# Kernel tuning notes

Hardware: AMD Instinct MI355X
Metric: run time of the kernel (lower is better)

## Reference

```python
import jax, jax.numpy as jnp
import numpy as np

EPS = 1e-5
SCALES = jnp.array([7.0, 7.0, 4.0], dtype=jnp.float32)  # (W, H, T) per source buffer
OUT_T, OUT_H, OUT_W = 3, 5, 5


def _roi_align3d(feat, start, end):
    """feat: [C,T,H,W]; start/end: [3] = (x, y, t). One sample per bin (bin center),
    trilinear interpolation, out-of-bounds -> 0 (standard ROIAlign convention)."""
    C, T, H, W = feat.shape
    dt = feat.dtype

    def centers(s, e, n):
        b = (e - s) / n
        return s + (jnp.arange(n, dtype=dt) + 0.5) * b

    xc = centers(start[0], end[0], OUT_W)  # [Wo]
    yc = centers(start[1], end[1], OUT_H)  # [Ho]
    tc = centers(start[2], end[2], OUT_T)  # [To]

    def prep(c, size):
        valid = ((c >= -1.0) & (c <= size)).astype(dt)
        c = jnp.clip(c, 0.0, size - 1)
        lo = jnp.floor(c).astype(jnp.int32)
        hi = jnp.minimum(lo + 1, size - 1)
        f = c - lo.astype(dt)
        return (lo, hi), ((1.0 - f) * valid, f * valid)

    ti, tw = prep(tc, T)
    yi, yw = prep(yc, H)
    xi, xw = prep(xc, W)

    out = jnp.zeros((C, OUT_T, OUT_H, OUT_W), dtype=dt)
    for a in range(2):
        for b in range(2):
            for c in range(2):
                g = feat[:, ti[a][:, None, None], yi[b][None, :, None], xi[c][None, None, :]]
                w = tw[a][:, None, None] * yw[b][None, :, None] * xw[c][None, None, :]
                out = out + g * w
    return out


def setup_inputs() -> dict:
    key = jax.random.key(0)
    k0, k1, k2 = jax.random.split(key, 3)
    B, C, T, H, W = 128, 1024, 4, 7, 7
    R = 256
    x = jax.random.normal(k0, (B, C, T, H, W), jnp.float32)
    w1 = jax.random.normal(k1, (R, C), jnp.float32) / np.sqrt(C).astype(np.float32)
    w2 = jax.random.normal(k2, (6, R), jnp.float32) / np.sqrt(R).astype(np.float32)
    return dict(
        x=x, w1=w1,
        g1=jnp.ones((R,), jnp.float32), b1=jnp.zeros((R,), jnp.float32),
        m1=jnp.zeros((R,), jnp.float32), v1=jnp.ones((R,), jnp.float32),
        w2=w2,
        g2=jnp.ones((6,), jnp.float32), b2=jnp.zeros((6,), jnp.float32),
        m2=jnp.zeros((6,), jnp.float32), v2=jnp.ones((6,), jnp.float32),
    )


def reference(x, w1, g1, b1, m1, v1, w2, g2, b2, m2, v2):
    # roi head: conv1x1x1 -> BN(eval) -> HSwish -> global avgpool -> conv1x1x1 -> BN(eval)
    h = jnp.einsum('bcthw,rc->brthw', x, w1)
    s1 = (g1 / jnp.sqrt(v1 + EPS))
    h = (h - m1[None, :, None, None, None]) * s1[None, :, None, None, None] + b1[None, :, None, None, None]
    h = h * jnp.clip(h + 3.0, 0.0, 6.0) * (1.0 / 6.0)  # HSwish
    h = h.mean(axis=(2, 3, 4))                          # AvgPool3d over full (T,H,W) -> [B,R]
    logits = h @ w2.T
    logits = (logits - m2) * (g2 / jnp.sqrt(v2 + EPS)) + b2  # [B,6]
    raw = jax.nn.sigmoid(logits)
    roi_start = 0.5 * raw[:, :3] * SCALES              # (x1,y1,t1)
    roi_end = (1.0 - 0.5 * raw[:, 3:]) * SCALES        # (x2,y2,t2)
    return jax.vmap(_roi_align3d)(x, roi_start, roi_end)  # [B,C,3,5,5]
```

## Files before the change

### kernel.cpp

```cpp
#include <hip/hip_runtime.h>

typedef __bf16 bf16x8 __attribute__((ext_vector_type(8)));
typedef float f32x4 __attribute__((ext_vector_type(4)));

#define EPS_F 1e-5f

__device__ __forceinline__ unsigned short f2bf(float f) {
    unsigned int u;
    __builtin_memcpy(&u, &f, 4);
    unsigned int r = (u + 0x7fffu + ((u >> 16) & 1u)) >> 16;
    return (unsigned short)r;
}

__global__ __launch_bounds__(256) void k_gemm_pool(
    const float* __restrict__ x,
    const float* __restrict__ w1,
    const float* __restrict__ g1,
    const float* __restrict__ b1,
    const float* __restrict__ m1,
    const float* __restrict__ v1,
    float* __restrict__ pooled)
{
    constexpr int LDK = 40;
    __shared__ unsigned short Alds[224 * LDK];
    __shared__ unsigned short Blds[64 * LDK];
    __shared__ float pool_lds[2][64];

    const int b   = blockIdx.x;
    const int r0  = blockIdx.y * 64;
    const int tid = threadIdx.x;
    const int wave = tid >> 6, lane = tid & 63;
    const int wn = wave >> 1, wm = wave & 1;
    const int q  = lane >> 4, ln = lane & 15;

    f32x4 acc[7][2];
#pragma unroll
    for (int i = 0; i < 7; i++)
#pragma unroll
        for (int j = 0; j < 2; j++) acc[i][j] = (f32x4){0.f, 0.f, 0.f, 0.f};

    const int c4 = tid / 28;
    const int p8 = tid % 28;

    for (int kc = 0; kc < 1024; kc += 32) {
        __syncthreads();
        {
            const int r  = tid >> 2;
            const int k8 = tid & 3;
            const float* wb = w1 + (size_t)(r0 + r) * 1024 + kc + k8 * 8;
            const float4 f0 = *(const float4*)wb;
            const float4 f1 = *(const float4*)(wb + 4);
            ushort4 o0, o1;
            o0.x = f2bf(f0.x); o0.y = f2bf(f0.y); o0.z = f2bf(f0.z); o0.w = f2bf(f0.w);
            o1.x = f2bf(f1.x); o1.y = f2bf(f1.y); o1.z = f2bf(f1.z); o1.w = f2bf(f1.w);
            *(ushort4*)&Blds[r * LDK + k8 * 8]     = o0;
            *(ushort4*)&Blds[r * LDK + k8 * 8 + 4] = o1;
        }
        if (tid < 224) {
            float rowv[4][8];
#pragma unroll
            for (int i = 0; i < 4; i++) {
                const int c = kc + c4 * 4 + i;
                const float* base = x + ((size_t)b * 1024 + c) * 196 + p8 * 8;
                if (p8 < 24) {
                    const float4 f0 = *(const float4*)base;
                    const float4 f1 = *(const float4*)(base + 4);
                    rowv[i][0] = f0.x; rowv[i][1] = f0.y; rowv[i][2] = f0.z; rowv[i][3] = f0.w;
                    rowv[i][4] = f1.x; rowv[i][5] = f1.y; rowv[i][6] = f1.z; rowv[i][7] = f1.w;
                } else if (p8 == 24) {
                    const float4 f0 = *(const float4*)base;
                    rowv[i][0] = f0.x; rowv[i][1] = f0.y; rowv[i][2] = f0.z; rowv[i][3] = f0.w;
                    rowv[i][4] = 0.f; rowv[i][5] = 0.f; rowv[i][6] = 0.f; rowv[i][7] = 0.f;
                } else {
#pragma unroll
                    for (int j = 0; j < 8; j++) rowv[i][j] = 0.f;
                }
            }
#pragma unroll
            for (int j = 0; j < 8; j++) {
                ushort4 o;
                o.x = f2bf(rowv[0][j]);
                o.y = f2bf(rowv[1][j]);
                o.z = f2bf(rowv[2][j]);
                o.w = f2bf(rowv[3][j]);
                *(ushort4*)&Alds[(p8 * 8 + j) * LDK + c4 * 4] = o;
            }
        }
        __syncthreads();
        bf16x8 bfr[2];
#pragma unroll
        for (int nt = 0; nt < 2; nt++)
            bfr[nt] = *(const bf16x8*)&Blds[(wn * 32 + nt * 16 + ln) * LDK + q * 8];
#pragma unroll
        for (int mi = 0; mi < 7; mi++) {
            const int mt = wm * 7 + mi;
            const bf16x8 af = *(const bf16x8*)&Alds[(mt * 16 + ln) * LDK + q * 8];
            acc[mi][0] = __builtin_amdgcn_mfma_f32_16x16x32_bf16(af, bfr[0], acc[mi][0], 0, 0, 0);
            acc[mi][1] = __builtin_amdgcn_mfma_f32_16x16x32_bf16(af, bfr[1], acc[mi][1], 0, 0, 0);
        }
    }

    float psum[2] = {0.f, 0.f};
#pragma unroll
    for (int nt = 0; nt < 2; nt++) {
        const int r = r0 + wn * 32 + nt * 16 + ln;
        const float s1 = g1[r] * rsqrtf(v1[r] + EPS_F);
        const float mu = m1[r];
        const float be = b1[r];
#pragma unroll
        for (int mi = 0; mi < 7; mi++) {
            const int mt = wm * 7 + mi;
#pragma unroll
            for (int i = 0; i < 4; i++) {
                const int m = mt * 16 + q * 4 + i;
                if (m < 196) {
                    float v = acc[mi][nt][i];
                    v = (v - mu) * s1 + be;
                    const float g = fminf(fmaxf(v + 3.f, 0.f), 6.f);
                    psum[nt] += v * g * (1.f / 6.f);
                }
            }
        }
    }
#pragma unroll
    for (int nt = 0; nt < 2; nt++) {
        psum[nt] += __shfl_xor(psum[nt], 16, 64);
        psum[nt] += __shfl_xor(psum[nt], 32, 64);
        if (lane < 16) pool_lds[wm][wn * 32 + nt * 16 + lane] = psum[nt];
    }
    __syncthreads();
    if (tid < 64)
        pooled[b * 256 + r0 + tid] =
            (pool_lds[0][tid] + pool_lds[1][tid]) * (1.f / 196.f);
}

__global__ __launch_bounds__(64) void k_logits(
    const float* __restrict__ pooled,
    const float* __restrict__ w2,
    const float* __restrict__ g2,
    const float* __restrict__ b2,
    const float* __restrict__ m2,
    const float* __restrict__ v2,
    float* __restrict__ roi)
{
    const int b = blockIdx.x, t = threadIdx.x;
    const float4 p4 = ((const float4*)(pooled + b * 256))[t];
    float part[6];
#pragma unroll
    for (int j = 0; j < 6; j++) {
        const float4 w = *(const float4*)(w2 + j * 256 + t * 4);
        part[j] = p4.x * w.x + p4.y * w.y + p4.z * w.z + p4.w * w.w;
    }
#pragma unroll
    for (int j = 0; j < 6; j++)
#pragma unroll
        for (int off = 32; off >= 1; off >>= 1)
            part[j] += __shfl_xor(part[j], off, 64);
    if (t == 0) {
        const float SC[3] = {7.f, 7.f, 4.f};
        float raw[6];
#pragma unroll
        for (int j = 0; j < 6; j++) {
            float l = part[j];
            const float s = g2[j] * rsqrtf(v2[j] + EPS_F);
            l = (l - m2[j]) * s + b2[j];
            raw[j] = 1.f / (1.f + expf(-l));
        }
#pragma unroll
        for (int d = 0; d < 3; d++) {
            roi[b * 6 + d]     = 0.5f * raw[d] * SC[d];
            roi[b * 6 + 3 + d] = (1.f - 0.5f * raw[3 + d]) * SC[d];
        }
    }
}

__global__ __launch_bounds__(256) void k_roi(
    const float* __restrict__ x,
    const float* __restrict__ roi,
    float* __restrict__ out)
{
    __shared__ int   slo[13], shi[13];
    __shared__ float sw0[13], sw1[13];
    const int b = blockIdx.x, c0 = blockIdx.y * 128;
    const int tid = threadIdx.x;
    if (tid < 13) {
        int i, n, size, sidx;
        if (tid < 3)      { i = tid;     n = 3; size = 4; sidx = 2; }
        else if (tid < 8) { i = tid - 3; n = 5; size = 7; sidx = 1; }
        else              { i = tid - 8; n = 5; size = 7; sidx = 0; }
        const float s = roi[b * 6 + sidx];
        const float e = roi[b * 6 + 3 + sidx];
        const float bsz = (e - s) / (float)n;
        float c = s + ((float)i + 0.5f) * bsz;
        const float valid = (c >= -1.f && c <= (float)size) ? 1.f : 0.f;
        c = fminf(fmaxf(c, 0.f), (float)(size - 1));
        const int lo = (int)floorf(c);
        const int hi = min(lo + 1, size - 1);
        const float f = c - (float)lo;
        slo[tid] = lo; shi[tid] = hi;
        sw0[tid] = (1.f - f) * valid; sw1[tid] = f * valid;
    }
    __syncthreads();
    for (int e = tid; e < 128 * 75; e += 256) {
        const int c  = c0 + e / 75;
        const int po = e % 75;
        const int to = po / 25, rem = po % 25, yo = rem / 5, xo = rem % 5;
        const int   tl = slo[to],      th = shi[to];
        const float tw0 = sw0[to],     tw1 = sw1[to];
        const int   yl = slo[3 + yo],  yh = shi[3 + yo];
        const float yw0 = sw0[3 + yo], yw1 = sw1[3 + yo];
        const int   xl = slo[8 + xo],  xh = shi[8 + xo];
        const float xw0 = sw0[8 + xo], xw1 = sw1[8 + xo];
        const float* base = x + ((size_t)b * 1024 + c) * 196;
        const float v =
            tw0 * (yw0 * (xw0 * base[tl * 49 + yl * 7 + xl] +
                          xw1 * base[tl * 49 + yl * 7 + xh]) +
                   yw1 * (xw0 * base[tl * 49 + yh * 7 + xl] +
                          xw1 * base[tl * 49 + yh * 7 + xh])) +
            tw1 * (yw0 * (xw0 * base[th * 49 + yl * 7 + xl] +
                          xw1 * base[th * 49 + yl * 7 + xh]) +
                   yw1 * (xw0 * base[th * 49 + yh * 7 + xl] +
                          xw1 * base[th * 49 + yh * 7 + xh]));
        out[((size_t)b * 1024 + c) * 75 + po] = v;
    }
}

extern "C" void kernel_launch(void* const* d_in, const int* in_sizes, int n_in,
                              void* d_out, int out_size, void* d_ws, size_t ws_size,
                              hipStream_t stream)
{
    const float* x  = (const float*)d_in[0];
    const float* w1 = (const float*)d_in[1];
    const float* g1 = (const float*)d_in[2];
    const float* b1 = (const float*)d_in[3];
    const float* m1 = (const float*)d_in[4];
    const float* v1 = (const float*)d_in[5];
    const float* w2 = (const float*)d_in[6];
    const float* g2 = (const float*)d_in[7];
    const float* b2 = (const float*)d_in[8];
    const float* m2 = (const float*)d_in[9];
    const float* v2 = (const float*)d_in[10];

    float* pooled = (float*)d_ws;
    float* roi    = pooled + 128 * 256;
    float* out    = (float*)d_out;

    k_gemm_pool<<<dim3(128, 4), 256, 0, stream>>>(x, w1, g1, b1, m1, v1, pooled);
    k_logits<<<128, 64, 0, stream>>>(pooled, w2, g2, b2, m2, v2, roi);
    k_roi<<<dim3(128, 8), 256, 0, stream>>>(x, roi, out);
}
```

Baseline: 268.0 us.

## Widen GEMM-pool block to 8 waves and stage ROI features through LDS

The GEMM+pool kernel moves from 4 to 8 waves per block. Each wave now owns one 16-column N tile instead of two, which halves the accumulator registers and splits the A/B staging loads into smaller per-thread float4 chunks. The ROI-align kernel now uses smaller 32-channel tiles. Each tile is loaded coalesced into LDS, and the 8 trilinear offsets and weights per output point are precomputed once per block, replacing scattered global gathers. The grid grows to 4096 ROI blocks, and the larger GEMM blocks may lower occupancy.

```diff
diff --git a/kernel.cpp b/kernel.cpp
--- a/kernel.cpp
+++ b/kernel.cpp
@@ -12,7 +12,7 @@
     return (unsigned short)r;
 }
 
-__global__ __launch_bounds__(256) void k_gemm_pool(
+__global__ __launch_bounds__(512) void k_gemm_pool(
     const float* __restrict__ x,
     const float* __restrict__ w1,
     const float* __restrict__ g1,
@@ -30,80 +30,66 @@
     const int r0  = blockIdx.y * 64;
     const int tid = threadIdx.x;
     const int wave = tid >> 6, lane = tid & 63;
-    const int wn = wave >> 1, wm = wave & 1;
+    const int wm = wave >> 2, wn = wave & 3;
     const int q  = lane >> 4, ln = lane & 15;
 
-    f32x4 acc[7][2];
-#pragma unroll
-    for (int i = 0; i < 7; i++)
-#pragma unroll
-        for (int j = 0; j < 2; j++) acc[i][j] = (f32x4){0.f, 0.f, 0.f, 0.f};
-
-    const int c4 = tid / 28;
-    const int p8 = tid % 28;
+    f32x4 acc[7];
+#pragma unroll
+    for (int i = 0; i < 7; i++) acc[i] = (f32x4){0.f, 0.f, 0.f, 0.f};
+
+    const int c4  = tid & 7;
+    const int p4  = tid >> 3;
+    const bool a_act = (p4 < 56);
+    const bool a_val = (p4 < 49);
+    const float* xb = x + (size_t)b * 1024 * 196 + p4 * 4;
+
+    const int rB = tid >> 3, k16 = tid & 7;
 
     for (int kc = 0; kc < 1024; kc += 32) {
         __syncthreads();
         {
-            const int r  = tid >> 2;
-            const int k8 = tid & 3;
-            const float* wb = w1 + (size_t)(r0 + r) * 1024 + kc + k8 * 8;
-            const float4 f0 = *(const float4*)wb;
-            const float4 f1 = *(const float4*)(wb + 4);
-            ushort4 o0, o1;
-            o0.x = f2bf(f0.x); o0.y = f2bf(f0.y); o0.z = f2bf(f0.z); o0.w = f2bf(f0.w);
-            o1.x = f2bf(f1.x); o1.y = f2bf(f1.y); o1.z = f2bf(f1.z); o1.w = f2bf(f1.w);
-            *(ushort4*)&Blds[r * LDK + k8 * 8]     = o0;
-            *(ushort4*)&Blds[r * LDK + k8 * 8 + 4] = o1;
-        }
-        if (tid < 224) {
-            float rowv[4][8];
-#pragma unroll
-            for (int i = 0; i < 4; i++) {
-                const int c = kc + c4 * 4 + i;
-                const float* base = x + ((size_t)b * 1024 + c) * 196 + p8 * 8;
-                if (p8 < 24) {
-                    const float4 f0 = *(const float4*)base;
-                    const float4 f1 = *(const float4*)(base + 4);
-                    rowv[i][0] = f0.x; rowv[i][1] = f0.y; rowv[i][2] = f0.z; rowv[i][3] = f0.w;
-                    rowv[i][4] = f1.x; rowv[i][5] = f1.y; rowv[i][6] = f1.z; rowv[i][7] = f1.w;
-                } else if (p8 == 24) {
-                    const float4 f0 = *(const float4*)base;
-                    rowv[i][0] = f0.x; rowv[i][1] = f0.y; rowv[i][2] = f0.z; rowv[i][3] = f0.w;
-                    rowv[i][4] = 0.f; rowv[i][5] = 0.f; rowv[i][6] = 0.f; rowv[i][7] = 0.f;
-                } else {
-#pragma unroll
-                    for (int j = 0; j < 8; j++) rowv[i][j] = 0.f;
+            const float4 f = *(const float4*)(w1 + (size_t)(r0 + rB) * 1024 + kc + k16 * 4);
+            ushort4 o;
+            o.x = f2bf(f.x); o.y = f2bf(f.y); o.z = f2bf(f.z); o.w = f2bf(f.w);
+            *(ushort4*)&Blds[rB * LDK + k16 * 4] = o;
+        }
+        if (a_act) {
+            float fv[4][4];
+            if (a_val) {
+#pragma unroll
+                for (int i = 0; i < 4; i++) {
+                    const float4 f = *(const float4*)(xb + (size_t)(kc + c4 * 4 + i) * 196);
+                    fv[i][0] = f.x; fv[i][1] = f.y; fv[i][2] = f.z; fv[i][3] = f.w;
                 }
+            } else {
+#pragma unroll
+                for (int i = 0; i < 4; i++)
+#pragma unroll
+                    for (int j = 0; j < 4; j++) fv[i][j] = 0.f;
             }
 #pragma unroll
-            for (int j = 0; j < 8; j++) {
+            for (int j = 0; j < 4; j++) {
                 ushort4 o;
-                o.x = f2bf(rowv[0][j]);
-                o.y = f2bf(rowv[1][j]);
-                o.z = f2bf(rowv[2][j]);
-                o.w = f2bf(rowv[3][j]);
-                *(ushort4*)&Alds[(p8 * 8 + j) * LDK + c4 * 4] = o;
+                o.x = f2bf(fv[0][j]);
+                o.y = f2bf(fv[1][j]);
+                o.z = f2bf(fv[2][j]);
+                o.w = f2bf(fv[3][j]);
+                *(ushort4*)&Alds[(p4 * 4 + j) * LDK + c4 * 4] = o;
             }
         }
         __syncthreads();
-        bf16x8 bfr[2];
-#pragma unroll
-        for (int nt = 0; nt < 2; nt++)
-            bfr[nt] = *(const bf16x8*)&Blds[(wn * 32 + nt * 16 + ln) * LDK + q * 8];
+        const bf16x8 bfr = *(const bf16x8*)&Blds[(wn * 16 + ln) * LDK + q * 8];
 #pragma unroll
         for (int mi = 0; mi < 7; mi++) {
             const int mt = wm * 7 + mi;
             const bf16x8 af = *(const bf16x8*)&Alds[(mt * 16 + ln) * LDK + q * 8];
-            acc[mi][0] = __builtin_amdgcn_mfma_f32_16x16x32_bf16(af, bfr[0], acc[mi][0], 0, 0, 0);
-            acc[mi][1] = __builtin_amdgcn_mfma_f32_16x16x32_bf16(af, bfr[1], acc[mi][1], 0, 0, 0);
-        }
-    }
-
-    float psum[2] = {0.f, 0.f};
-#pragma unroll
-    for (int nt = 0; nt < 2; nt++) {
-        const int r = r0 + wn * 32 + nt * 16 + ln;
+            acc[mi] = __builtin_amdgcn_mfma_f32_16x16x32_bf16(af, bfr, acc[mi], 0, 0, 0);
+        }
+    }
+
+    float psum = 0.f;
+    {
+        const int r = r0 + wn * 16 + ln;
         const float s1 = g1[r] * rsqrtf(v1[r] + EPS_F);
         const float mu = m1[r];
         const float be = b1[r];
@@ -114,20 +100,17 @@
             for (int i = 0; i < 4; i++) {
                 const int m = mt * 16 + q * 4 + i;
                 if (m < 196) {
-                    float v = acc[mi][nt][i];
+                    float v = acc[mi][i];
                     v = (v - mu) * s1 + be;
                     const float g = fminf(fmaxf(v + 3.f, 0.f), 6.f);
-                    psum[nt] += v * g * (1.f / 6.f);
+                    psum += v * g * (1.f / 6.f);
                 }
             }
         }
     }
-#pragma unroll
-    for (int nt = 0; nt < 2; nt++) {
-        psum[nt] += __shfl_xor(psum[nt], 16, 64);
-        psum[nt] += __shfl_xor(psum[nt], 32, 64);
-        if (lane < 16) pool_lds[wm][wn * 32 + nt * 16 + lane] = psum[nt];
-    }
+    psum += __shfl_xor(psum, 16, 64);
+    psum += __shfl_xor(psum, 32, 64);
+    if (lane < 16) pool_lds[wm][wn * 16 + lane] = psum;
     __syncthreads();
     if (tid < 64)
         pooled[b * 256 + r0 + tid] =
@@ -174,54 +157,80 @@
     }
 }
 
+__device__ __forceinline__ void prep1(float s, float e, int n, int size, int i,
+                                      int& lo, int& hi, float& w0, float& w1)
+{
+    const float bsz = (e - s) / (float)n;
+    float c = s + ((float)i + 0.5f) * bsz;
+    const float valid = (c >= -1.f && c <= (float)size) ? 1.f : 0.f;
+    c = fminf(fmaxf(c, 0.f), (float)(size - 1));
+    lo = (int)floorf(c);
+    hi = min(lo + 1, size - 1);
+    const float f = c - (float)lo;
+    w0 = (1.f - f) * valid;
+    w1 = f * valid;
+}
+
 __global__ __launch_bounds__(256) void k_roi(
     const float* __restrict__ x,
     const float* __restrict__ roi,
     float* __restrict__ out)
 {
-    __shared__ int   slo[13], shi[13];
-    __shared__ float sw0[13], sw1[13];
-    const int b = blockIdx.x, c0 = blockIdx.y * 128;
+    __shared__ float xs[32 * 200];
+    __shared__ int   soff[8][80];
+    __shared__ float swt[8][80];
+
+    const int b = blockIdx.x, c0 = blockIdx.y * 32;
     const int tid = threadIdx.x;
-    if (tid < 13) {
-        int i, n, size, sidx;
-        if (tid < 3)      { i = tid;     n = 3; size = 4; sidx = 2; }
-        else if (tid < 8) { i = tid - 3; n = 5; size = 7; sidx = 1; }
-        else              { i = tid - 8; n = 5; size = 7; sidx = 0; }
-        const float s = roi[b * 6 + sidx];
-        const float e = roi[b * 6 + 3 + sidx];
-        const float bsz = (e - s) / (float)n;
-        float c = s + ((float)i + 0.5f) * bsz;
-        const float valid = (c >= -1.f && c <= (float)size) ? 1.f : 0.f;
-        c = fminf(fmaxf(c, 0.f), (float)(size - 1));
-        const int lo = (int)floorf(c);
-        const int hi = min(lo + 1, size - 1);
-        const float f = c - (float)lo;
-        slo[tid] = lo; shi[tid] = hi;
-        sw0[tid] = (1.f - f) * valid; sw1[tid] = f * valid;
+
+    const float* xb = x + ((size_t)b * 1024 + c0) * 196;
+#pragma unroll
+    for (int k = 0; k < 7; k++) {
+        const int i4 = tid + k * 256;
+        if (i4 < 1568) {
+            const int c = i4 / 49, pq = i4 % 49;
+            const float4 v = *(const float4*)(xb + c * 196 + pq * 4);
+            *(float4*)&xs[c * 200 + pq * 4] = v;
+        }
+    }
+    if (tid < 75) {
+        const int po = tid;
+        const int to = po / 25, rem = po % 25, yo = rem / 5, xo = rem % 5;
+        const float sx = roi[b * 6 + 0], ex = roi[b * 6 + 3];
+        const float sy = roi[b * 6 + 1], ey = roi[b * 6 + 4];
+        const float st = roi[b * 6 + 2], et = roi[b * 6 + 5];
+        int tl, th, yl, yh, xl, xh;
+        float tw0, tw1, yw0, yw1, xw0, xw1;
+        prep1(st, et, 3, 4, to, tl, th, tw0, tw1);
+        prep1(sy, ey, 5, 7, yo, yl, yh, yw0, yw1);
+        prep1(sx, ex, 5, 7, xo, xl, xh, xw0, xw1);
+#pragma unroll
+        for (int s = 0; s < 8; s++) {
+            const int   ti = (s & 4) ? th : tl;
+            const int   yi = (s & 2) ? yh : yl;
+            const int   xi = (s & 1) ? xh : xl;
+            const float w = ((s & 4) ? tw1 : tw0) *
+                            ((s & 2) ? yw1 : yw0) *
+                            ((s & 1) ? xw1 : xw0);
+            soff[s][po] = ti * 49 + yi * 7 + xi;
+            swt[s][po]  = w;
+        }
     }
     __syncthreads();
-    for (int e = tid; e < 128 * 75; e += 256) {
-        const int c  = c0 + e / 75;
-        const int po = e % 75;
-        const int to = po / 25, rem = po % 25, yo = rem / 5, xo = rem % 5;
-        const int   tl = slo[to],      th = shi[to];
-        const float tw0 = sw0[to],     tw1 = sw1[to];
-        const int   yl = slo[3 + yo],  yh = shi[3 + yo];
-        const float yw0 = sw0[3 + yo], yw1 = sw1[3 + yo];
-        const int   xl = slo[8 + xo],  xh = shi[8 + xo];
-        const float xw0 = sw0[8 + xo], xw1 = sw1[8 + xo];
-        const float* base = x + ((size_t)b * 1024 + c) * 196;
-        const float v =
-            tw0 * (yw0 * (xw0 * base[tl * 49 + yl * 7 + xl] +
-                          xw1 * base[tl * 49 + yl * 7 + xh]) +
-                   yw1 * (xw0 * base[tl * 49 + yh * 7 + xl] +
-                          xw1 * base[tl * 49 + yh * 7 + xh])) +
-            tw1 * (yw0 * (xw0 * base[th * 49 + yl * 7 + xl] +
-                          xw1 * base[th * 49 + yl * 7 + xh]) +
-                   yw1 * (xw0 * base[th * 49 + yh * 7 + xl] +
-                          xw1 * base[th * 49 + yh * 7 + xh]));
-        out[((size_t)b * 1024 + c) * 75 + po] = v;
+
+    const size_t obase = ((size_t)b * 1024 + c0) * 75;
+#pragma unroll
+    for (int k = 0; k < 10; k++) {
+        const int e = tid + k * 256;
+        if (e < 2400) {
+            const int c = e / 75, po = e % 75;
+            const float* row = &xs[c * 200];
+            float v = 0.f;
+#pragma unroll
+            for (int s = 0; s < 8; s++)
+                v += swt[s][po] * row[soff[s][po]];
+            out[obase + e] = v;
+        }
     }
 }
 
@@ -245,7 +254,7 @@
     float* roi    = pooled + 128 * 256;
     float* out    = (float*)d_out;
 
-    k_gemm_pool<<<dim3(128, 4), 256, 0, stream>>>(x, w1, g1, b1, m1, v1, pooled);
+    k_gemm_pool<<<dim3(128, 4), 512, 0, stream>>>(x, w1, g1, b1, m1, v1, pooled);
     k_logits<<<128, 64, 0, stream>>>(pooled, w2, g2, b2, m2, v2, roi);
-    k_roi<<<dim3(128, 8), 256, 0, stream>>>(x, roi, out);
-}
+    k_roi<<<dim3(128, 32), 256, 0, stream>>>(x, roi, out);
+}
```

Result: faster. 239.3 us (-10.7%).
